# Optimization experiments

Hardware: AMD Instinct MI355X
Metric: run time of the kernel (lower is better)

## Reference

```python
import jax, jax.numpy as jnp
import numpy as np

# ---- static config (mirrors PaCoVoxelLoss init) ----
NUM_QUERIES = 20
FACTOR = 64
NUM_GT = 12
K_NEIGHBORS = 8          # repulsion.num_neighbors
REP_EPS = 1e-12          # repulsion.epsilon
BANDWIDTH = 0.03         # repulsion.kernel_bandwidth
RADIUS = 0.07            # repulsion.radius
ALPHA_PARAM = 0.5
BETA_CHAMFER = 20.0
W_CLS, W_REP, W_CH1, W_CH2 = 1.0, 1.0, 1.0, 1.0
PAD_COST = 1e6           # pad value to square the rectangular assignment problem


def _hungarian(cost):
    # Jonker-Volgenant / e-maxx shortest augmenting path; cost: (n, n) float64.
    # Returns col_to_row: for each column j, the row assigned to it.
    n = cost.shape[0]
    INF = 1e18
    u = np.zeros(n + 1); v = np.zeros(n + 1)
    p = np.zeros(n + 1, dtype=np.int64)
    way = np.zeros(n + 1, dtype=np.int64)
    for i in range(1, n + 1):
        p[0] = i; j0 = 0
        minv = np.full(n + 1, INF)
        used = np.zeros(n + 1, dtype=bool)
        while True:
            used[j0] = True
            i0 = p[j0]; delta = INF; j1 = 0
            for j in range(1, n + 1):
                if not used[j]:
                    cur = cost[i0 - 1, j - 1] - u[i0] - v[j]
                    if cur < minv[j]:
                        minv[j] = cur; way[j] = j0
                    if minv[j] < delta:
                        delta = minv[j]; j1 = j
            for j in range(n + 1):
                if used[j]:
                    u[p[j]] += delta; v[j] -= delta
                else:
                    minv[j] -= delta
            j0 = j1
            if p[j0] == 0:
                break
        while j0 != 0:
            j1 = way[j0]; p[j0] = p[j1]; j0 = j1
    return p[1:] - 1


def _match(cost_np):
    # cost_np: (B, Q, P) with P <= Q -> rows (B, P): pred row matched to each gt col.
    Bn, Qn, Pn = cost_np.shape
    rows = np.zeros((Bn, Pn), dtype=np.int64)
    for b in range(Bn):
        sq = np.full((Qn, Qn), PAD_COST, dtype=np.float64)
        sq[:, :Pn] = cost_np[b].astype(np.float64)
        rows[b] = _hungarian(sq)[:Pn]
    return rows


def _gather_q(A, rows):
    # A: (B, Q, P), rows: (B, P) -> A[b, rows[b,p], p] : (B, P)
    return jnp.take_along_axis(A, rows[:, None, :], axis=1)[:, 0, :]


def _bce_logits(x, t):
    return jnp.maximum(x, 0.0) - x * t + jnp.log1p(jnp.exp(-jnp.abs(x)))


def _cost_terms(pred_normals, pred_distances, gt_normals, gt_distances, points, gt_masks):
    mask_f = gt_masks.astype(points.dtype)           # (B, P, N)
    cnt = mask_f.sum(-1)                             # (B, P)
    # |points . n_q - d_q| for all query planes: (B, Q, N)
    pp = jnp.abs(jnp.einsum('bnd,bqd->bqn', points, pred_normals) - pred_distances[:, :, None])
    cham_raw = jnp.einsum('bqn,bpn->bqp', pp, mask_f) / jnp.maximum(cnt, 1.0)[:, None, :]
    has = (cnt > 0)[:, None, :]                      # (B, 1, P)
    normal_sim = 1.0 - jnp.abs(jnp.einsum('bqd,bpd->bqp', pred_normals, gt_normals))
    dist_diff = jnp.abs(pred_distances[:, :, None] - gt_distances[:, None, :])
    cost = normal_sim + 0.5 * dist_diff + 5.0 * jnp.where(has, cham_raw, 1.0)
    return cost, cham_raw, normal_sim, dist_diff, has


def _losses(pred_logits, pred_normals, pred_distances, gt_normals, gt_distances,
            points, reconstructed_points, gt, gt_masks, rows):
    _, cham_raw, normal_sim, dist_diff, has = _cost_terms(
        pred_normals, pred_distances, gt_normals, gt_distances, points, gt_masks)

    # classification loss: target 1 at matched pred rows
    Qn = pred_logits.shape[1]
    cls_target = jax.nn.one_hot(rows, Qn, dtype=pred_logits.dtype).sum(axis=1)  # (B, Q)
    cls_loss = _bce_logits(pred_logits, cls_target).mean()

    # param loss over matched pairs (mean over P matches, mean over B)
    param_loss = (_gather_q(normal_sim, rows).mean(-1) + _gather_q(dist_diff, rows).mean(-1)).mean()

    # pvd chamfer: point-to-plane term, zero for empty masks, /P /B
    pvd_chamfer = _gather_q(jnp.where(has, cham_raw, 0.0), rows).mean()

    # repulsion loss on per-query point groups
    Bn = reconstructed_points.shape[0]
    rp = reconstructed_points.reshape(Bn, NUM_QUERIES, FACTOR, 3)
    d2 = jnp.sum((rp[:, :, :, None, :] - rp[:, :, None, :, :]) ** 2, axis=-1)  # (B,Q,F,F)
    _, idx = jax.lax.top_k(-d2, K_NEIGHBORS)       # k nearest incl. self
    dn = jnp.maximum(jnp.take_along_axis(d2, idx[..., 1:], axis=-1), REP_EPS)  # (B,Q,F,k-1)
    w = jnp.exp(-dn / BANDWIDTH ** 2)
    rep = jnp.maximum(jnp.mean((RADIUS - jnp.sqrt(dn)) * w, axis=(2, 3)), 0.0).mean()

    # fine-grained chamfer (L1 and L2) between reconstructed and gt clouds
    diff = reconstructed_points[:, :, None, :] - gt[:, None, :, :]  # (B, M, G, 3)
    d1 = jnp.abs(diff).sum(-1)
    d2c = (diff ** 2).sum(-1)
    ch1 = (0.5 * (d1.min(axis=2).mean(axis=1) + d1.min(axis=1).mean(axis=1))).mean()
    ch2 = (0.5 * (d2c.min(axis=2).mean(axis=1) + d2c.min(axis=1).mean(axis=1))).mean()

    total = (W_CLS * cls_loss + ALPHA_PARAM * param_loss + BETA_CHAMFER * pvd_chamfer
             + W_REP * rep + W_CH1 * ch1 + W_CH2 * ch2)
    return total


def setup_inputs() -> dict:
    key = jax.random.key(0)
    ks = jax.random.split(key, 10)
    B, Q, P, N, G = 8, NUM_QUERIES, NUM_GT, 4096, 2048

    def unit(k, shape):
        v = jax.random.normal(k, shape, dtype=jnp.float32)
        return v / jnp.linalg.norm(v, axis=-1, keepdims=True)

    return {
        'pred_logits': jax.random.normal(ks[0], (B, Q), dtype=jnp.float32),
        'pred_normals': unit(ks[1], (B, Q, 3)),
        'pred_distances': jax.random.normal(ks[2], (B, Q), dtype=jnp.float32),
        'gt_normals': unit(ks[3], (B, P, 3)),
        'gt_distances': jax.random.normal(ks[4], (B, P), dtype=jnp.float32),
        'gt_masks': jax.random.bernoulli(ks[5], 0.3, (B, P, N)),
        'points': jax.random.normal(ks[6], (B, N, 3), dtype=jnp.float32),
        'reconstructed_points': 0.5 * jax.random.normal(ks[7], (B, Q * FACTOR, 3), dtype=jnp.float32),
        'gt': jax.random.normal(ks[8], (B, G, 3), dtype=jnp.float32),
        'gt_index': jax.random.randint(ks[9], (B, G), 0, P, dtype=jnp.int64) if jax.config.jax_enable_x64 else jax.random.randint(ks[9], (B, G), 0, P, dtype=jnp.int32),
    }


def reference(pred_logits, pred_normals, pred_distances, gt_normals, gt_distances,
              points, reconstructed_points, gt, gt_masks, gt_index):
    cost = _cost_terms(pred_normals, pred_distances, gt_normals, gt_distances, points, gt_masks)[0]
    rows = jnp.asarray(_match(np.asarray(cost)))  # Hungarian (host, like scipy in original)
    return _losses(pred_logits, pred_normals, pred_distances, gt_normals, gt_distances,
                   points, reconstructed_points, gt, gt_masks, rows)
```

## Files before the change

kernel.cpp:

```cpp
#include <hip/hip_runtime.h>
#include <math.h>

#define Bn 8
#define Qn 20
#define Pn 12
#define Nn 4096
#define Gn 2048
#define Mn 1280
#define Fn 64
#define KNB 7
#define SA 8
#define SB 5
#define DONE_TARGET 113


__device__ __forceinline__ float aread(float* p) { return atomicAdd(p, 0.0f); }

__device__ __forceinline__ void contribute(float* acc, int* done, float* out) {
    __threadfence();
    int old = atomicAdd(done, 1);
    if (old == DONE_TARGET - 1) {
        __threadfence();
        float a0 = aread(&acc[0]);
        float a1 = aread(&acc[1]);
        float a2 = aread(&acc[2]);
        float a3 = aread(&acc[3]);
        float a4 = aread(&acc[4]);
        float a5 = aread(&acc[5]);
        out[0] = a0 + 0.5f * a1 + 20.f * a2 + a3 + a4 + a5;
    }
}

__device__ __forceinline__ int rdlane_i(int v, int l) {
    return __builtin_amdgcn_readlane(v, l);
}
__device__ __forceinline__ float rdlane_f(float v, int l) {
    return __int_as_float(__builtin_amdgcn_readlane(__float_as_int(v), l));
}
__device__ __forceinline__ unsigned wave_min_u32(unsigned x) {
    unsigned t;
    t = (unsigned)__builtin_amdgcn_update_dpp((int)0xFFFFFFFF, (int)x, 0x111, 0xF, 0xF, false);
    x = t < x ? t : x;
    t = (unsigned)__builtin_amdgcn_update_dpp((int)0xFFFFFFFF, (int)x, 0x112, 0xF, 0xF, false);
    x = t < x ? t : x;
    t = (unsigned)__builtin_amdgcn_update_dpp((int)0xFFFFFFFF, (int)x, 0x114, 0xF, 0xF, false);
    x = t < x ? t : x;
    t = (unsigned)__builtin_amdgcn_update_dpp((int)0xFFFFFFFF, (int)x, 0x118, 0xF, 0xF, false);
    x = t < x ? t : x;
    t = (unsigned)__builtin_amdgcn_update_dpp((int)0xFFFFFFFF, (int)x, 0x142, 0xF, 0xF, false);
    x = t < x ? t : x;
    t = (unsigned)__builtin_amdgcn_update_dpp((int)0xFFFFFFFF, (int)x, 0x143, 0xF, 0xF, false);
    x = t < x ? t : x;
    return x;
}

__global__ void mega1_kernel(const float* __restrict__ pred_normals,
                             const float* __restrict__ pred_distances,
                             const float* __restrict__ gt_normals,
                             const float* __restrict__ gt_distances,
                             const float* __restrict__ points,
                             const int*   __restrict__ gt_masks,
                             const float* __restrict__ recon,
                             const float* __restrict__ gt,
                             float* __restrict__ ws) {
    __shared__ __align__(16) float smem[2 * Pn * 256];
    const int blk = blockIdx.x;
    const int tid = threadIdx.x;

    float* cham = ws;
    float* ns   = ws + 1920;
    float* dd   = ws + 3840;
    float* cost = ws + 5760;
    float* cnt  = ws + 7680;
    float* acc  = ws + 7776;
    float* rep_part = ws + 7808;
    float* pmA1 = ws + 8192;
    float* pmA2 = ws + 90112;
    float* pmB1 = ws + 172032;
    float* pmB2 = ws + 253952;

    if (blk < 160) {
        if (blk == 0 && tid < 8) acc[tid] = 0.f;
        const int b = blk / Qn, q = blk % Qn;
        const float nx = pred_normals[(b * Qn + q) * 3 + 0];
        const float ny = pred_normals[(b * Qn + q) * 3 + 1];
        const float nz = pred_normals[(b * Qn + q) * 3 + 2];
        const float dq = pred_distances[b * Qn + q];

        float accs[Pn], accw[Pn];
#pragma unroll
        for (int p = 0; p < Pn; ++p) { accs[p] = 0.f; accw[p] = 0.f; }

        const float* ptb = points + (size_t)b * Nn * 3;
        const int*   mb  = gt_masks + (size_t)b * Pn * Nn;

        for (int n = tid; n < Nn; n += 256) {
            float px = ptb[n * 3 + 0], py = ptb[n * 3 + 1], pz = ptb[n * 3 + 2];
            float pp = fabsf(px * nx + py * ny + pz * nz - dq);
#pragma unroll
            for (int p = 0; p < Pn; ++p) {
                float m = (float)mb[(size_t)p * Nn + n];
                accs[p] += pp * m;
                accw[p] += m;
            }
        }
#pragma unroll
        for (int p = 0; p < Pn; ++p) {
            smem[p * 256 + tid] = accs[p];
            smem[(p + Pn) * 256 + tid] = accw[p];
        }
        __syncthreads();
        for (int off = 128; off > 0; off >>= 1) {
            if (tid < off) {
#pragma unroll
                for (int r = 0; r < 2 * Pn; ++r) smem[r * 256 + tid] += smem[r * 256 + tid + off];
            }
            __syncthreads();
        }
        if (tid < Pn) {
            const int p = tid;
            float c  = smem[(p + Pn) * 256];
            float cv = smem[p * 256] / fmaxf(c, 1.f);
            float gnx = gt_normals[(b * Pn + p) * 3 + 0];
            float gny = gt_normals[(b * Pn + p) * 3 + 1];
            float gnz = gt_normals[(b * Pn + p) * 3 + 2];
            float nsim = 1.f - fabsf(nx * gnx + ny * gny + nz * gnz);
            float ddv  = fabsf(dq - gt_distances[b * Pn + p]);
            int idx = (b * Qn + q) * Pn + p;
            cham[idx] = cv;
            ns[idx]   = nsim;
            dd[idx]   = ddv;
            cost[idx] = nsim + 0.5f * ddv + 5.f * ((c > 0.f) ? cv : 1.f);
            if (q == 0) cnt[b * Pn + p] = c;
        }
    } else if (blk < 200) {
        const int wave = tid >> 6, lane = tid & 63;
        const int g = (blk - 160) * 4 + wave;
        float* xs = smem + wave * 192;
        float* ys = xs + 64;
        float* zs = xs + 128;
        const float* base = recon + (size_t)g * Fn * 3;
        xs[lane] = base[lane * 3 + 0];
        ys[lane] = base[lane * 3 + 1];
        zs[lane] = base[lane * 3 + 2];
        float best[KNB];
#pragma unroll
        for (int k = 0; k < KNB; ++k) best[k] = 3.4e38f;
        const float xi = xs[lane], yi = ys[lane], zi = zs[lane];
        for (int j = 0; j < Fn; ++j) {
            float dx = xi - xs[j], dy = yi - ys[j], dz = zi - zs[j];
            float d2 = dx * dx + dy * dy + dz * dz;
            d2 = (j == lane) ? 3.4e38f : d2;
#pragma unroll
            for (int k = 0; k < KNB; ++k) {
                float lo = fminf(best[k], d2);
                float hi = fmaxf(best[k], d2);
                best[k] = lo;
                d2 = hi;
            }
        }
        float sum = 0.f;
#pragma unroll
        for (int k = 0; k < KNB; ++k) {
            float dn = fmaxf(best[k], 1e-12f);
            float w  = expf(-dn / (0.03f * 0.03f));
            sum += (0.07f - sqrtf(dn)) * w;
        }
        for (int off = 32; off > 0; off >>= 1) sum += __shfl_down(sum, off);
        if (lane == 0) rep_part[g] = fmaxf(sum / (float)(Fn * KNB), 0.f);
    } else {
        int cblk = blk - 200;
        float4* tile = reinterpret_cast<float4*>(smem);
        float x, y, z;
        const float* inner;
        float *o1, *o2;
        int idx;
        if (cblk < 40 * SA) {
            int s = cblk % SA, ob = cblk / SA;
            idx = ob * 256 + tid;
            int b = idx / Mn;
            x = recon[idx * 3 + 0]; y = recon[idx * 3 + 1]; z = recon[idx * 3 + 2];
            inner = gt + ((size_t)b * Gn + s * 256) * 3;
            o1 = pmA1 + s * (Bn * Mn); o2 = pmA2 + s * (Bn * Mn);
        } else {
            cblk -= 40 * SA;
            int s = cblk % SB, ob = cblk / SB;
            idx = ob * 256 + tid;
            int b = idx / Gn;
            x = gt[idx * 3 + 0]; y = gt[idx * 3 + 1]; z = gt[idx * 3 + 2];
            inner = recon + ((size_t)b * Mn + s * 256) * 3;
            o1 = pmB1 + s * (Bn * Gn); o2 = pmB2 + s * (Bn * Gn);
        }
        {
            const float* ip = inner + tid * 3;
            float4 tv;
            tv.x = ip[0]; tv.y = ip[1]; tv.z = ip[2]; tv.w = 0.f;
            tile[tid] = tv;
        }
        __syncthreads();
        float m1 = 3.4e38f, m2 = 3.4e38f;
#pragma unroll 4
        for (int j = 0; j < 256; ++j) {
            float4 tv = tile[j];
            float dx = x - tv.x, dy = y - tv.y, dz = z - tv.z;
            float d1 = fabsf(dx) + fabsf(dy) + fabsf(dz);
            float d2 = dx * dx + dy * dy + dz * dz;
            m1 = fminf(m1, d1); m2 = fminf(m2, d2);
        }
        o1[idx] = m1; o2[idx] = m2;
    }
}

__global__ void finale_kernel(const float* __restrict__ pred_logits,
                              float* __restrict__ ws, float* __restrict__ out) {
    const int blk = blockIdx.x;
    const int tid = threadIdx.x;

    float* cham = ws;
    float* ns   = ws + 1920;
    float* dd   = ws + 3840;
    float* cost = ws + 5760;
    float* cnt  = ws + 7680;
    float* acc  = ws + 7776;
    int*   done = (int*)(ws + 7782);
    float* rep_part = ws + 7808;
    float* pmA1 = ws + 8192;
    float* pmA2 = ws + 90112;
    float* pmB1 = ws + 172032;
    float* pmB2 = ws + 253952;

    if (blk < 8) {
        if (tid >= 64) return;
        const int b = blk;
        const int t = tid;
        const int col = t;
        const bool isCol = (col >= 1 && col <= Qn);

        float cr[Pn];
#pragma unroll
        for (int k = 0; k < Pn; ++k) cr[k] = 0.f;
        if (isCol) {
            const float* cb = cost + ((size_t)b * Qn + (col - 1)) * Pn;
#pragma unroll
            for (int k = 0; k < Pn; ++k) cr[k] = cb[k];
        }

        float v = 0.f, u = 0.f, minv = 0.f;
        int way = 0, p = 0;

        for (int i = 1; i <= Pn; ++i) {
            minv = 1e30f;
            bool used = false;
            bool rowInPath = false;
            int j0s = 0;
            while (true) {
                if (col == j0s) used = true;
                int i0s = (j0s == 0) ? i : rdlane_i(p, j0s);
                if (t == i0s) rowInPath = true;
                float u_i0 = rdlane_f(u, i0s);
                const int bs = i0s - 1;
                float l10 = (bs & 1) ? cr[1]  : cr[0];
                float l11 = (bs & 1) ? cr[3]  : cr[2];
                float l12 = (bs & 1) ? cr[5]  : cr[4];
                float l13 = (bs & 1) ? cr[7]  : cr[6];
                float l14 = (bs & 1) ? cr[9]  : cr[8];
                float l15 = (bs & 1) ? cr[11] : cr[10];
                float l20 = (bs & 2) ? l11 : l10;
                float l21 = (bs & 2) ? l13 : l12;
                float l22 = (bs & 2) ? l15 : l14;
                float cij = (bs >= 8) ? l22 : ((bs >= 4) ? l21 : l20);
                if (isCol && !used) {
                    float cur = cij - u_i0 - v;
                    if (cur < minv) { minv = cur; way = j0s; }
                }
                float mv = (isCol && !used) ? minv : 1e30f;
                unsigned kb = __float_as_uint(mv);
                kb = ((int)kb < 0) ? ~kb : (kb | 0x80000000u);
                kb = (kb & ~31u) | (unsigned)(col & 31);
                unsigned kmin = (unsigned)rdlane_i((int)wave_min_u32(kb), 63);
                int j1 = (int)(kmin & 31u);
                float delta = rdlane_f(minv, j1);
                if (used || col == 0) v -= delta;
                else if (isCol)       minv -= delta;
                if (rowInPath)        u += delta;
                j0s = j1;
                int pj0 = rdlane_i(p, j0s);
                if (pj0 == 0) break;
            }
            while (j0s != 0) {
                int wj = rdlane_i(way, j0s);
                int pw = (wj == 0) ? i : rdlane_i(p, wj);
                if (col == j0s) p = pw;
                j0s = wj;
            }
        }

        float cls = 0.f, par = 0.f, pvd = 0.f;
        if (isCol) {
            float x = pred_logits[b * Qn + (col - 1)];
            float tgt = (p > 0) ? 1.f : 0.f;
            cls = fmaxf(x, 0.f) - x * tgt + log1pf(expf(-fabsf(x)));
            if (p > 0) {
                int idx = (b * Qn + (col - 1)) * Pn + (p - 1);
                par = ns[idx] + dd[idx];
                pvd = (cnt[b * Pn + (p - 1)] > 0.f) ? cham[idx] : 0.f;
            }
        }
        for (int off = 32; off > 0; off >>= 1) {
            cls += __shfl_down(cls, off);
            par += __shfl_down(par, off);
            pvd += __shfl_down(pvd, off);
        }
        if (t == 0) {
            atomicAdd(&acc[0], cls / (float)(Bn * Qn));
            atomicAdd(&acc[1], par / (float)(Bn * Pn));
            atomicAdd(&acc[2], pvd / (float)(Bn * Pn));
            contribute(acc, done, out);
        }
        return;
    }

    __shared__ float s1[256], s2[256];
    const int cblk = blk - 8;
    float c1 = 0.f, c2 = 0.f;
    if (cblk < 40) {
        int idx = cblk * 256 + tid;
        float m1 = 3.4e38f, m2 = 3.4e38f;
#pragma unroll
        for (int s = 0; s < SA; ++s) {
            m1 = fminf(m1, pmA1[s * (Bn * Mn) + idx]);
            m2 = fminf(m2, pmA2[s * (Bn * Mn) + idx]);
        }
        c1 = m1 * (0.5f / (float)(Bn * Mn));
        c2 = m2 * (0.5f / (float)(Bn * Mn));
    } else if (cblk < 104) {
        int idx = (cblk - 40) * 256 + tid;
        float m1 = 3.4e38f, m2 = 3.4e38f;
#pragma unroll
        for (int s = 0; s < SB; ++s) {
            m1 = fminf(m1, pmB1[s * (Bn * Gn) + idx]);
            m2 = fminf(m2, pmB2[s * (Bn * Gn) + idx]);
        }
        c1 = m1 * (0.5f / (float)(Bn * Gn));
        c2 = m2 * (0.5f / (float)(Bn * Gn));
    } else {
        c1 = (tid < Bn * Qn) ? rep_part[tid] / (float)(Bn * Qn) : 0.f;
    }
    s1[tid] = c1; s2[tid] = c2;
    __syncthreads();
    for (int off = 128; off > 0; off >>= 1) {
        if (tid < off) { s1[tid] += s1[tid + off]; s2[tid] += s2[tid + off]; }
        __syncthreads();
    }
    if (tid == 0) {
        if (cblk < 104) {
            atomicAdd(&acc[4], s1[0]);
            atomicAdd(&acc[5], s2[0]);
        } else {
            atomicAdd(&acc[3], s1[0]);
        }
        contribute(acc, done, out);
    }
}

extern "C" void kernel_launch(void* const* d_in, const int* in_sizes, int n_in,
                              void* d_out, int out_size, void* d_ws, size_t ws_size,
                              hipStream_t stream) {
    const float* pred_logits    = (const float*)d_in[0];
    const float* pred_normals   = (const float*)d_in[1];
    const float* pred_distances = (const float*)d_in[2];
    const float* gt_normals     = (const float*)d_in[3];
    const float* gt_distances   = (const float*)d_in[4];
    const int*   gt_masks       = (const int*)d_in[5];
    const float* points         = (const float*)d_in[6];
    const float* recon          = (const float*)d_in[7];
    const float* gt             = (const float*)d_in[8];

    mega1_kernel<<<840, 256, 0, stream>>>(pred_normals, pred_distances, gt_normals,
                                          gt_distances, points, gt_masks, recon, gt,
                                          (float*)d_ws);
    finale_kernel<<<113, 256, 0, stream>>>(pred_logits, (float*)d_ws, (float*)d_out);
}
```

Baseline: 109.0 us.

## Fuse producer and finale kernels into one launch with a global spin barrier

Merges the two kernel launches into a single kernel. Every block publishes its results with agent-scope atomic stores and bumps a completion counter, and the first 113 blocks spin on that counter before running the Hungarian matching and reduction phase. This removes one kernel launch and the gap between kernels. The spin-wait assumes the 113 waiting blocks never starve the remaining producer blocks of residency, and the ws counters are reset relative to a base value. Producer blocks with low indices may also have to wait on slow chamfer blocks.

Result: slower. 113.2 us (+3.9%).

```diff
diff --git a/kernel.cpp b/kernel.cpp
--- a/kernel.cpp
+++ b/kernel.cpp
@@ -11,16 +11,48 @@
 #define KNB 7
 #define SA 8
 #define SB 5
-#define DONE_TARGET 113
+#define NPROD 840
+#define NFIN 113
+#define SCOPE_AGENT __HIP_MEMORY_SCOPE_AGENT
 
 
 __device__ __forceinline__ float aread(float* p) { return atomicAdd(p, 0.0f); }
-
-__device__ __forceinline__ void contribute(float* acc, int* done, float* out) {
-    __threadfence();
-    int old = atomicAdd(done, 1);
-    if (old == DONE_TARGET - 1) {
-        __threadfence();
+__device__ __forceinline__ void ast(float* p, float v) {
+    __hip_atomic_store(p, v, __ATOMIC_RELAXED, SCOPE_AGENT);
+}
+__device__ __forceinline__ float ald(const float* p) {
+    return __hip_atomic_load(p, __ATOMIC_RELAXED, SCOPE_AGENT);
+}
+
+__device__ __forceinline__ int rdlane_i(int v, int l) {
+    return __builtin_amdgcn_readlane(v, l);
+}
+__device__ __forceinline__ float rdlane_f(float v, int l) {
+    return __int_as_float(__builtin_amdgcn_readlane(__float_as_int(v), l));
+}
+__device__ __forceinline__ unsigned wave_min_u32(unsigned x) {
+    unsigned t;
+    t = (unsigned)__builtin_amdgcn_update_dpp((int)0xFFFFFFFF, (int)x, 0x111, 0xF, 0xF, false);
+    x = t < x ? t : x;
+    t = (unsigned)__builtin_amdgcn_update_dpp((int)0xFFFFFFFF, (int)x, 0x112, 0xF, 0xF, false);
+    x = t < x ? t : x;
+    t = (unsigned)__builtin_amdgcn_update_dpp((int)0xFFFFFFFF, (int)x, 0x114, 0xF, 0xF, false);
+    x = t < x ? t : x;
+    t = (unsigned)__builtin_amdgcn_update_dpp((int)0xFFFFFFFF, (int)x, 0x118, 0xF, 0xF, false);
+    x = t < x ? t : x;
+    t = (unsigned)__builtin_amdgcn_update_dpp((int)0xFFFFFFFF, (int)x, 0x142, 0xF, 0xF, false);
+    x = t < x ? t : x;
+    t = (unsigned)__builtin_amdgcn_update_dpp((int)0xFFFFFFFF, (int)x, 0x143, 0xF, 0xF, false);
+    x = t < x ? t : x;
+    return x;
+}
+
+__device__ __forceinline__ void finpost(float* ws, float* out, unsigned init) {
+    unsigned* doneP = (unsigned*)(ws + 7782);
+    unsigned* c2P   = (unsigned*)(ws + 7784);
+    float* acc = ws + 7776;
+    unsigned old = __hip_atomic_fetch_add(c2P, 1u, __ATOMIC_ACQ_REL, SCOPE_AGENT);
+    if (old - init == (unsigned)(NFIN - 1)) {
         float a0 = aread(&acc[0]);
         float a1 = aread(&acc[1]);
         float a2 = aread(&acc[2]);
@@ -28,33 +60,13 @@
         float a4 = aread(&acc[4]);
         float a5 = aread(&acc[5]);
         out[0] = a0 + 0.5f * a1 + 20.f * a2 + a3 + a4 + a5;
-    }
-}
-
-__device__ __forceinline__ int rdlane_i(int v, int l) {
-    return __builtin_amdgcn_readlane(v, l);
-}
-__device__ __forceinline__ float rdlane_f(float v, int l) {
-    return __int_as_float(__builtin_amdgcn_readlane(__float_as_int(v), l));
-}
-__device__ __forceinline__ unsigned wave_min_u32(unsigned x) {
-    unsigned t;
-    t = (unsigned)__builtin_amdgcn_update_dpp((int)0xFFFFFFFF, (int)x, 0x111, 0xF, 0xF, false);
-    x = t < x ? t : x;
-    t = (unsigned)__builtin_amdgcn_update_dpp((int)0xFFFFFFFF, (int)x, 0x112, 0xF, 0xF, false);
-    x = t < x ? t : x;
-    t = (unsigned)__builtin_amdgcn_update_dpp((int)0xFFFFFFFF, (int)x, 0x114, 0xF, 0xF, false);
-    x = t < x ? t : x;
-    t = (unsigned)__builtin_amdgcn_update_dpp((int)0xFFFFFFFF, (int)x, 0x118, 0xF, 0xF, false);
-    x = t < x ? t : x;
-    t = (unsigned)__builtin_amdgcn_update_dpp((int)0xFFFFFFFF, (int)x, 0x142, 0xF, 0xF, false);
-    x = t < x ? t : x;
-    t = (unsigned)__builtin_amdgcn_update_dpp((int)0xFFFFFFFF, (int)x, 0x143, 0xF, 0xF, false);
-    x = t < x ? t : x;
-    return x;
-}
-
-__global__ void mega1_kernel(const float* __restrict__ pred_normals,
+        __hip_atomic_store(doneP, init, __ATOMIC_RELAXED, SCOPE_AGENT);
+        __hip_atomic_store(c2P,   init, __ATOMIC_RELAXED, SCOPE_AGENT);
+    }
+}
+
+__global__ void fused_kernel(const float* __restrict__ pred_logits,
+                             const float* __restrict__ pred_normals,
                              const float* __restrict__ pred_distances,
                              const float* __restrict__ gt_normals,
                              const float* __restrict__ gt_distances,
@@ -62,7 +74,8 @@
                              const int*   __restrict__ gt_masks,
                              const float* __restrict__ recon,
                              const float* __restrict__ gt,
-                             float* __restrict__ ws) {
+                             float* __restrict__ ws,
+                             float* __restrict__ out) {
     __shared__ __align__(16) float smem[2 * Pn * 256];
     const int blk = blockIdx.x;
     const int tid = threadIdx.x;
@@ -73,14 +86,18 @@
     float* cost = ws + 5760;
     float* cnt  = ws + 7680;
     float* acc  = ws + 7776;
+    unsigned* doneP = (unsigned*)(ws + 7782);
+    unsigned* baseP = (unsigned*)(ws + 7783);
     float* rep_part = ws + 7808;
     float* pmA1 = ws + 8192;
     float* pmA2 = ws + 90112;
     float* pmB1 = ws + 172032;
     float* pmB2 = ws + 253952;
 
+    const unsigned init = __hip_atomic_load(baseP, __ATOMIC_RELAXED, SCOPE_AGENT);
+
     if (blk < 160) {
-        if (blk == 0 && tid < 8) acc[tid] = 0.f;
+        if (blk == 0 && tid < 6) ast(&acc[tid], 0.f);
         const int b = blk / Qn, q = blk % Qn;
         const float nx = pred_normals[(b * Qn + q) * 3 + 0];
         const float ny = pred_normals[(b * Qn + q) * 3 + 1];
@@ -127,11 +144,11 @@
             float nsim = 1.f - fabsf(nx * gnx + ny * gny + nz * gnz);
             float ddv  = fabsf(dq - gt_distances[b * Pn + p]);
             int idx = (b * Qn + q) * Pn + p;
-            cham[idx] = cv;
-            ns[idx]   = nsim;
-            dd[idx]   = ddv;
-            cost[idx] = nsim + 0.5f * ddv + 5.f * ((c > 0.f) ? cv : 1.f);
-            if (q == 0) cnt[b * Pn + p] = c;
+            ast(&cham[idx], cv);
+            ast(&ns[idx],   nsim);
+            ast(&dd[idx],   ddv);
+            ast(&cost[idx], nsim + 0.5f * ddv + 5.f * ((c > 0.f) ? cv : 1.f));
+            if (q == 0) ast(&cnt[b * Pn + p], c);
         }
     } else if (blk < 200) {
         const int wave = tid >> 6, lane = tid & 63;
@@ -167,7 +184,7 @@
             sum += (0.07f - sqrtf(dn)) * w;
         }
         for (int off = 32; off > 0; off >>= 1) sum += __shfl_down(sum, off);
-        if (lane == 0) rep_part[g] = fmaxf(sum / (float)(Fn * KNB), 0.f);
+        if (lane == 0) ast(&rep_part[g], fmaxf(sum / (float)(Fn * KNB), 0.f));
     } else {
         int cblk = blk - 200;
         float4* tile = reinterpret_cast<float4*>(smem);
@@ -207,159 +224,157 @@
             float d2 = dx * dx + dy * dy + dz * dz;
             m1 = fminf(m1, d1); m2 = fminf(m2, d2);
         }
-        o1[idx] = m1; o2[idx] = m2;
-    }
-}
-
-__global__ void finale_kernel(const float* __restrict__ pred_logits,
-                              float* __restrict__ ws, float* __restrict__ out) {
-    const int blk = blockIdx.x;
-    const int tid = threadIdx.x;
-
-    float* cham = ws;
-    float* ns   = ws + 1920;
-    float* dd   = ws + 3840;
-    float* cost = ws + 5760;
-    float* cnt  = ws + 7680;
-    float* acc  = ws + 7776;
-    int*   done = (int*)(ws + 7782);
-    float* rep_part = ws + 7808;
-    float* pmA1 = ws + 8192;
-    float* pmA2 = ws + 90112;
-    float* pmB1 = ws + 172032;
-    float* pmB2 = ws + 253952;
+        ast(&o1[idx], m1);
+        ast(&o2[idx], m2);
+    }
+
+    __syncthreads();
+    if (tid == 0) __hip_atomic_fetch_add(doneP, 1u, __ATOMIC_RELEASE, SCOPE_AGENT);
+
+    if (blk >= NFIN) return;
+
+    if (tid == 0) {
+        while (__hip_atomic_load(doneP, __ATOMIC_RELAXED, SCOPE_AGENT) - init != (unsigned)NPROD)
+            __builtin_amdgcn_s_sleep(2);
+        (void)__hip_atomic_load(doneP, __ATOMIC_ACQUIRE, SCOPE_AGENT);
+    }
+    __syncthreads();
 
     if (blk < 8) {
-        if (tid >= 64) return;
-        const int b = blk;
-        const int t = tid;
-        const int col = t;
-        const bool isCol = (col >= 1 && col <= Qn);
-
-        float cr[Pn];
-#pragma unroll
-        for (int k = 0; k < Pn; ++k) cr[k] = 0.f;
-        if (isCol) {
-            const float* cb = cost + ((size_t)b * Qn + (col - 1)) * Pn;
-#pragma unroll
-            for (int k = 0; k < Pn; ++k) cr[k] = cb[k];
-        }
-
-        float v = 0.f, u = 0.f, minv = 0.f;
-        int way = 0, p = 0;
-
-        for (int i = 1; i <= Pn; ++i) {
-            minv = 1e30f;
-            bool used = false;
-            bool rowInPath = false;
-            int j0s = 0;
-            while (true) {
-                if (col == j0s) used = true;
-                int i0s = (j0s == 0) ? i : rdlane_i(p, j0s);
-                if (t == i0s) rowInPath = true;
-                float u_i0 = rdlane_f(u, i0s);
-                const int bs = i0s - 1;
-                float l10 = (bs & 1) ? cr[1]  : cr[0];
-                float l11 = (bs & 1) ? cr[3]  : cr[2];
-                float l12 = (bs & 1) ? cr[5]  : cr[4];
-                float l13 = (bs & 1) ? cr[7]  : cr[6];
-                float l14 = (bs & 1) ? cr[9]  : cr[8];
-                float l15 = (bs & 1) ? cr[11] : cr[10];
-                float l20 = (bs & 2) ? l11 : l10;
-                float l21 = (bs & 2) ? l13 : l12;
-                float l22 = (bs & 2) ? l15 : l14;
-                float cij = (bs >= 8) ? l22 : ((bs >= 4) ? l21 : l20);
-                if (isCol && !used) {
-                    float cur = cij - u_i0 - v;
-                    if (cur < minv) { minv = cur; way = j0s; }
+        if (tid < 64) {
+            const int b = blk;
+            const int t = tid;
+            const int col = t;
+            const bool isCol = (col >= 1 && col <= Qn);
+
+            float cr[Pn];
+#pragma unroll
+            for (int k = 0; k < Pn; ++k) cr[k] = 0.f;
+            if (isCol) {
+                const float* cb = cost + ((size_t)b * Qn + (col - 1)) * Pn;
+#pragma unroll
+                for (int k = 0; k < Pn; ++k) cr[k] = ald(&cb[k]);
+            }
+
+            float v = 0.f, u = 0.f, minv = 0.f;
+            int way = 0, p = 0;
+
+            for (int i = 1; i <= Pn; ++i) {
+                minv = 1e30f;
+                bool used = false;
+                bool rowInPath = false;
+                int j0s = 0;
+                while (true) {
+                    if (col == j0s) used = true;
+                    int i0s = (j0s == 0) ? i : rdlane_i(p, j0s);
+                    if (t == i0s) rowInPath = true;
+                    float u_i0 = rdlane_f(u, i0s);
+                    const int bs = i0s - 1;
+                    float l10 = (bs & 1) ? cr[1]  : cr[0];
+                    float l11 = (bs & 1) ? cr[3]  : cr[2];
+                    float l12 = (bs & 1) ? cr[5]  : cr[4];
+                    float l13 = (bs & 1) ? cr[7]  : cr[6];
+                    float l14 = (bs & 1) ? cr[9]  : cr[8];
+                    float l15 = (bs & 1) ? cr[11] : cr[10];
+                    float l20 = (bs & 2) ? l11 : l10;
+                    float l21 = (bs & 2) ? l13 : l12;
+                    float l22 = (bs & 2) ? l15 : l14;
+                    float cij = (bs >= 8) ? l22 : ((bs >= 4) ? l21 : l20);
+                    if (isCol && !used) {
+                        float cur = cij - u_i0 - v;
+                        if (cur < minv) { minv = cur; way = j0s; }
+                    }
+                    float mv = (isCol && !used) ? minv : 1e30f;
+                    unsigned kb = __float_as_uint(mv);
+                    kb = ((int)kb < 0) ? ~kb : (kb | 0x80000000u);
+                    kb = (kb & ~31u) | (unsigned)(col & 31);
+                    unsigned kmin = (unsigned)rdlane_i((int)wave_min_u32(kb), 63);
+                    int j1 = (int)(kmin & 31u);
+                    float delta = rdlane_f(minv, j1);
+                    if (used || col == 0) v -= delta;
+                    else if (isCol)       minv -= delta;
+                    if (rowInPath)        u += delta;
+                    j0s = j1;
+                    int pj0 = rdlane_i(p, j0s);
+                    if (pj0 == 0) break;
                 }
-                float mv = (isCol && !used) ? minv : 1e30f;
-                unsigned kb = __float_as_uint(mv);
-                kb = ((int)kb < 0) ? ~kb : (kb | 0x80000000u);
-                kb = (kb & ~31u) | (unsigned)(col & 31);
-                unsigned kmin = (unsigned)rdlane_i((int)wave_min_u32(kb), 63);
-                int j1 = (int)(kmin & 31u);
-                float delta = rdlane_f(minv, j1);
-                if (used || col == 0) v -= delta;
-                else if (isCol)       minv -= delta;
-                if (rowInPath)        u += delta;
-                j0s = j1;
-                int pj0 = rdlane_i(p, j0s);
-                if (pj0 == 0) break;
-            }
-            while (j0s != 0) {
-                int wj = rdlane_i(way, j0s);
-                int pw = (wj == 0) ? i : rdlane_i(p, wj);
-                if (col == j0s) p = pw;
-                j0s = wj;
-            }
-        }
-
-        float cls = 0.f, par = 0.f, pvd = 0.f;
-        if (isCol) {
-            float x = pred_logits[b * Qn + (col - 1)];
-            float tgt = (p > 0) ? 1.f : 0.f;
-            cls = fmaxf(x, 0.f) - x * tgt + log1pf(expf(-fabsf(x)));
-            if (p > 0) {
-                int idx = (b * Qn + (col - 1)) * Pn + (p - 1);
-                par = ns[idx] + dd[idx];
-                pvd = (cnt[b * Pn + (p - 1)] > 0.f) ? cham[idx] : 0.f;
-            }
-        }
-        for (int off = 32; off > 0; off >>= 1) {
-            cls += __shfl_down(cls, off);
-            par += __shfl_down(par, off);
-            pvd += __shfl_down(pvd, off);
-        }
-        if (t == 0) {
-            atomicAdd(&acc[0], cls / (float)(Bn * Qn));
-            atomicAdd(&acc[1], par / (float)(Bn * Pn));
-            atomicAdd(&acc[2], pvd / (float)(Bn * Pn));
-            contribute(acc, done, out);
+                while (j0s != 0) {
+                    int wj = rdlane_i(way, j0s);
+                    int pw = (wj == 0) ? i : rdlane_i(p, wj);
+                    if (col == j0s) p = pw;
+                    j0s = wj;
+                }
+            }
+
+            float cls = 0.f, par = 0.f, pvd = 0.f;
+            if (isCol) {
+                float x = pred_logits[b * Qn + (col - 1)];
+                float tgt = (p > 0) ? 1.f : 0.f;
+                cls = fmaxf(x, 0.f) - x * tgt + log1pf(expf(-fabsf(x)));
+                if (p > 0) {
+                    int idx = (b * Qn + (col - 1)) * Pn + (p - 1);
+                    par = ald(&ns[idx]) + ald(&dd[idx]);
+                    pvd = (ald(&cnt[b * Pn + (p - 1)]) > 0.f) ? ald(&cham[idx]) : 0.f;
+                }
+            }
+            for (int off = 32; off > 0; off >>= 1) {
+                cls += __shfl_down(cls, off);
+                par += __shfl_down(par, off);
+                pvd += __shfl_down(pvd, off);
+            }
+            if (t == 0) {
+                atomicAdd(&acc[0], cls / (float)(Bn * Qn));
+                atomicAdd(&acc[1], par / (float)(Bn * Pn));
+                atomicAdd(&acc[2], pvd / (float)(Bn * Pn));
+                finpost(ws, out, init);
+            }
         }
         return;
     }
 
-    __shared__ float s1[256], s2[256];
-    const int cblk = blk - 8;
-    float c1 = 0.f, c2 = 0.f;
-    if (cblk < 40) {
-        int idx = cblk * 256 + tid;
-        float m1 = 3.4e38f, m2 = 3.4e38f;
-#pragma unroll
-        for (int s = 0; s < SA; ++s) {
-            m1 = fminf(m1, pmA1[s * (Bn * Mn) + idx]);
-            m2 = fminf(m2, pmA2[s * (Bn * Mn) + idx]);
-        }
-        c1 = m1 * (0.5f / (float)(Bn * Mn));
-        c2 = m2 * (0.5f / (float)(Bn * Mn));
-    } else if (cblk < 104) {
-        int idx = (cblk - 40) * 256 + tid;
-        float m1 = 3.4e38f, m2 = 3.4e38f;
-#pragma unroll
-        for (int s = 0; s < SB; ++s) {
-            m1 = fminf(m1, pmB1[s * (Bn * Gn) + idx]);
-            m2 = fminf(m2, pmB2[s * (Bn * Gn) + idx]);
-        }
-        c1 = m1 * (0.5f / (float)(Bn * Gn));
-        c2 = m2 * (0.5f / (float)(Bn * Gn));
-    } else {
-        c1 = (tid < Bn * Qn) ? rep_part[tid] / (float)(Bn * Qn) : 0.f;
-    }
-    s1[tid] = c1; s2[tid] = c2;
-    __syncthreads();
-    for (int off = 128; off > 0; off >>= 1) {
-        if (tid < off) { s1[tid] += s1[tid + off]; s2[tid] += s2[tid + off]; }
+    {
+        float* s1 = smem;
+        float* s2 = smem + 256;
+        const int cblk = blk - 8;
+        float c1 = 0.f, c2 = 0.f;
+        if (cblk < 40) {
+            int idx = cblk * 256 + tid;
+            float m1 = 3.4e38f, m2 = 3.4e38f;
+#pragma unroll
+            for (int s = 0; s < SA; ++s) {
+                m1 = fminf(m1, ald(&pmA1[s * (Bn * Mn) + idx]));
+                m2 = fminf(m2, ald(&pmA2[s * (Bn * Mn) + idx]));
+            }
+            c1 = m1 * (0.5f / (float)(Bn * Mn));
+            c2 = m2 * (0.5f / (float)(Bn * Mn));
+        } else if (cblk < 104) {
+            int idx = (cblk - 40) * 256 + tid;
+            float m1 = 3.4e38f, m2 = 3.4e38f;
+#pragma unroll
+            for (int s = 0; s < SB; ++s) {
+                m1 = fminf(m1, ald(&pmB1[s * (Bn * Gn) + idx]));
+                m2 = fminf(m2, ald(&pmB2[s * (Bn * Gn) + idx]));
+            }
+            c1 = m1 * (0.5f / (float)(Bn * Gn));
+            c2 = m2 * (0.5f / (float)(Bn * Gn));
+        } else {
+            c1 = (tid < Bn * Qn) ? ald(&rep_part[tid]) / (float)(Bn * Qn) : 0.f;
+        }
+        s1[tid] = c1; s2[tid] = c2;
         __syncthreads();
-    }
-    if (tid == 0) {
-        if (cblk < 104) {
-            atomicAdd(&acc[4], s1[0]);
-            atomicAdd(&acc[5], s2[0]);
-        } else {
-            atomicAdd(&acc[3], s1[0]);
-        }
-        contribute(acc, done, out);
+        for (int off = 128; off > 0; off >>= 1) {
+            if (tid < off) { s1[tid] += s1[tid + off]; s2[tid] += s2[tid + off]; }
+            __syncthreads();
+        }
+        if (tid == 0) {
+            if (cblk < 104) {
+                atomicAdd(&acc[4], s1[0]);
+                atomicAdd(&acc[5], s2[0]);
+            } else {
+                atomicAdd(&acc[3], s1[0]);
+            }
+            finpost(ws, out, init);
+        }
     }
 }
 
@@ -376,8 +391,7 @@
     const float* recon          = (const float*)d_in[7];
     const float* gt             = (const float*)d_in[8];
 
-    mega1_kernel<<<840, 256, 0, stream>>>(pred_normals, pred_distances, gt_normals,
-                                          gt_distances, points, gt_masks, recon, gt,
-                                          (float*)d_ws);
-    finale_kernel<<<113, 256, 0, stream>>>(pred_logits, (float*)d_ws, (float*)d_out);
-}
+    fused_kernel<<<NPROD, 256, 0, stream>>>(pred_logits, pred_normals, pred_distances,
+                                            gt_normals, gt_distances, points, gt_masks,
+                                            recon, gt, (float*)d_ws, (float*)d_out);
+}
```
